# Kernel tuning notes

Hardware: AMD Instinct MI355X
Metric: run time of the kernel (lower is better)

The kernel has to match this reference:

```python
import jax, jax.numpy as jnp
import numpy as np

B, C, H, W = 64, 128, 32, 32
GROUPS = 32
EPS = 1e-6
SCALE = 0.044194173824159216  # 1/sqrt(512), as hardcoded in the torch module


def setup_inputs() -> dict:
    key = jax.random.key(0)
    ks = jax.random.split(key, 12)
    s = 1.0 / np.sqrt(C)
    return {
        "x": jax.random.normal(ks[0], (B, C, H, W), dtype=jnp.float32),
        "gn_w": jax.random.normal(ks[1], (C,), dtype=jnp.float32) * 0.02 + 1.0,
        "gn_b": jax.random.normal(ks[2], (C,), dtype=jnp.float32) * 0.02,
        "wq": jax.random.uniform(ks[3], (C, C), jnp.float32, -s, s),
        "bq": jax.random.uniform(ks[4], (C,), jnp.float32, -s, s),
        "wk": jax.random.uniform(ks[5], (C, C), jnp.float32, -s, s),
        "bk": jax.random.uniform(ks[6], (C,), jnp.float32, -s, s),
        "wv": jax.random.uniform(ks[7], (C, C), jnp.float32, -s, s),
        "bv": jax.random.uniform(ks[8], (C,), jnp.float32, -s, s),
        "wo": jax.random.uniform(ks[9], (C, C), jnp.float32, -s, s),
        "bo": jax.random.uniform(ks[10], (C,), jnp.float32, -s, s),
    }


def reference(x, gn_w, gn_b, wq, bq, wk, bk, wv, bv, wo, bo):
    b = x.shape[0]
    res = x
    # GroupNorm(32 groups, 128 channels): normalize over (channels_per_group, H, W)
    xg = x.reshape(b, GROUPS, C // GROUPS, H * W)
    mean = xg.mean(axis=(2, 3), keepdims=True)
    var = xg.var(axis=(2, 3), keepdims=True)
    xn = (xg - mean) * jax.lax.rsqrt(var + EPS)
    xn = xn.reshape(b, C, H, W) * gn_w[:, None, None] + gn_b[:, None, None]
    # flatten spatial -> sequence: [b, S=1024, C=128]
    t = xn.reshape(b, C, H * W).transpose(0, 2, 1)
    q = t @ wq.T + bq
    k = t @ wk.T + bk
    v = t @ wv.T + bv
    att = jnp.einsum('bsc,btc->bst', q, k) * SCALE  # [b, S, S]
    att = jax.nn.softmax(att, axis=-1)
    o = jnp.einsum('bst,btc->bsc', att, v)
    o = o @ wo.T + bo
    out = o.transpose(0, 2, 1).reshape(b, C, H, W) + res
    return out
```

## Files before the change

kernel.cpp:

```cpp
#include <hip/hip_runtime.h>
#include <hip/hip_bf16.h>

#define BATCH 64
#define CCH 128
#define SEQ 1024
#define NG 32
#define EPSV 1e-6f
#define SCALEV 0.044194173824159216f

typedef short v8s __attribute__((ext_vector_type(8)));
typedef short v4s __attribute__((ext_vector_type(4)));
typedef float v4f __attribute__((ext_vector_type(4)));
typedef int   v4i __attribute__((ext_vector_type(4)));
typedef unsigned short us;

__device__ __forceinline__ us f2bf(float f) {
    __hip_bfloat16 h = __float2bfloat16(f);
    return *reinterpret_cast<us*>(&h);
}

#define MFMA16(a, b, c) __builtin_amdgcn_mfma_f32_16x16x32_bf16(a, b, c, 0, 0, 0)

__device__ __forceinline__ void gld_lds16(const us* g, us* l) {
    __builtin_amdgcn_global_load_lds(
        (const __attribute__((address_space(1))) void*)g,
        (__attribute__((address_space(3))) void*)l, 16, 0, 0);
}

__global__ void prep_gn(const float* __restrict__ wq, const float* __restrict__ wk,
                        const float* __restrict__ wv, const float* __restrict__ wo,
                        us* wbf, const float* __restrict__ x,
                        float* meanr, float* rstdr) {
    int tid = threadIdx.x;
    if (blockIdx.x < 256) {
        int i = blockIdx.x * 256 + tid;
        const float* srcs[4] = {wq, wk, wv, wo};
        wbf[i] = f2bf(srcs[i >> 14][i & 16383]);
        return;
    }
    int bg = blockIdx.x - 256;
    const float4* p = (const float4*)(x + (size_t)bg * (4 * SEQ));
    float s1 = 0.f, s2 = 0.f;
    #pragma unroll
    for (int i = 0; i < 4; i++) {
        float4 v = p[i * 256 + tid];
        s1 += v.x + v.y + v.z + v.w;
        s2 += v.x * v.x + v.y * v.y + v.z * v.z + v.w * v.w;
    }
    #pragma unroll
    for (int off = 32; off; off >>= 1) {
        s1 += __shfl_down(s1, off);
        s2 += __shfl_down(s2, off);
    }
    __shared__ float a1[4], a2[4];
    int w = tid >> 6, l = tid & 63;
    if (l == 0) { a1[w] = s1; a2[w] = s2; }
    __syncthreads();
    if (tid == 0) {
        float t1 = a1[0] + a1[1] + a1[2] + a1[3];
        float t2 = a2[0] + a2[1] + a2[2] + a2[3];
        float mean = t1 * (1.0f / (4 * SEQ));
        float var  = t2 * (1.0f / (4 * SEQ)) - mean * mean;
        meanr[bg] = mean;
        rstdr[bg] = rsqrtf(var + EPSV);
    }
}

__global__ __launch_bounds__(256, 2) void qkv_kernel(
    const float* __restrict__ x, const float* __restrict__ gn_w,
    const float* __restrict__ gn_b, const float* __restrict__ meanr,
    const float* __restrict__ rstdr, const us* __restrict__ wbf,
    const float* __restrict__ bq, const float* __restrict__ bk,
    const float* __restrict__ bv,
    us* Q, us* K, us* Vt)
{
    __shared__ us tls[64 * 136];
    __shared__ float sa[CCH], sb[CCH];
    int b  = blockIdx.x >> 4;
    int s0 = (blockIdx.x & 15) * 64;
    int tid = threadIdx.x;
    const float* xb = x + (size_t)b * CCH * SEQ;

    if (tid < CCH) {
        int g = tid >> 2;
        float rs = rstdr[b * NG + g];
        float mu = meanr[b * NG + g];
        float a_ = rs * gn_w[tid];
        sa[tid] = a_;
        sb[tid] = gn_b[tid] - mu * a_;
    }
    __syncthreads();

    #pragma unroll
    for (int rep = 0; rep < 8; rep++) {
        int idx = rep * 256 + tid;
        int c = idx >> 4, s4 = idx & 15;
        float4 v = *(const float4*)&xb[c * SEQ + s0 + s4 * 4];
        float a_ = sa[c], b_ = sb[c];
        int sbase = s4 * 4;
        tls[(sbase + 0) * 136 + c] = f2bf(v.x * a_ + b_);
        tls[(sbase + 1) * 136 + c] = f2bf(v.y * a_ + b_);
        tls[(sbase + 2) * 136 + c] = f2bf(v.z * a_ + b_);
        tls[(sbase + 3) * 136 + c] = f2bf(v.w * a_ + b_);
    }
    __syncthreads();

    int w = tid >> 6, lane = tid & 63;
    int m = lane & 15, quad = lane >> 4;

    v8s bfr[6][4];
    float bias[6];
    #pragma unroll
    for (int t = 0; t < 6; t++) {
        int T = w * 6 + t;
        int o = T >> 3, ct = T & 7;
        const us* wmat = wbf + o * 16384;
        #pragma unroll
        for (int ch = 0; ch < 4; ch++)
            bfr[t][ch] = *(const v8s*)&wmat[(ct * 16 + m) * 128 + ch * 32 + quad * 8];
        const float* bb = (o == 0) ? bq : (o == 1) ? bk : bv;
        bias[t] = bb[ct * 16 + m];
    }

    us* Qb = Q + (size_t)b * SEQ * CCH;
    us* Kb = K + (size_t)b * SEQ * CCH;
    us* Vb = Vt + (size_t)b * CCH * SEQ;

    #pragma unroll
    for (int st = 0; st < 4; st++) {
        v8s a[4];
        #pragma unroll
        for (int ch = 0; ch < 4; ch++)
            a[ch] = *(const v8s*)&tls[(st * 16 + m) * 136 + ch * 32 + quad * 8];
        int srow = s0 + st * 16 + quad * 4;
        #pragma unroll
        for (int t = 0; t < 6; t++) {
            int T = w * 6 + t;
            int o = T >> 3, ct = T & 7;
            v4f acc = {0,0,0,0};
            #pragma unroll
            for (int ch = 0; ch < 4; ch++)
                acc = MFMA16(a[ch], bfr[t][ch], acc);
            int col = ct * 16 + m;
            if (o < 2) {
                us* dst = (o == 0) ? Qb : Kb;
                #pragma unroll
                for (int r = 0; r < 4; r++)
                    dst[(size_t)(srow + r) * 128 + col] = f2bf(acc[r] + bias[t]);
            } else {
                v4s pk;
                #pragma unroll
                for (int r = 0; r < 4; r++) pk[r] = (short)f2bf(acc[r] + bias[t]);
                *(v4s*)&Vb[(size_t)col * SEQ + srow] = pk;
            }
        }
    }
}

__global__ __launch_bounds__(256, 2) void attn_kernel(
    const us* __restrict__ Q, const us* __restrict__ K,
    const us* __restrict__ Vt, const us* __restrict__ wbo,
    const float* __restrict__ bo, const float* __restrict__ x,
    float* __restrict__ out)
{
    __shared__ char smem_raw[65536];

    int i = blockIdx.x;
    int b  = (i & 7) * 8 + ((i >> 3) & 7);
    int qt = i >> 6;
    int tid = threadIdx.x;
    int w = tid >> 6, lane = tid & 63;
    int m = lane & 15, quad = lane >> 4;
    int qrow0 = qt * 64 + w * 16;
    const us* Qb = Q + (size_t)b * SEQ * CCH;
    const us* Kb = K + (size_t)b * SEQ * CCH;
    const us* Vb = Vt + (size_t)b * CCH * SEQ;

    v8s aq[4];
    #pragma unroll
    for (int ch = 0; ch < 4; ch++)
        aq[ch] = *(const v8s*)&Qb[(size_t)(qrow0 + m) * 128 + ch * 32 + quad * 8];

    v4f oacc[8];
    #pragma unroll
    for (int ct = 0; ct < 8; ct++) oacc[ct] = (v4f){0, 0, 0, 0};
    float lrun = 0.f;

    const us* kg[4]; const us* vg[4];
    int jb = w * 4;
    #pragma unroll
    for (int j4 = 0; j4 < 4; j4++) {
        int j = jb + j4;
        int kr = 4 * j + (lane >> 4);
        kg[j4] = Kb + (size_t)kr * 128 + ((lane & 15) ^ (kr & 15)) * 8;
        int vc = 8 * j + (lane >> 3);
        vg[j4] = Vb + (size_t)vc * SEQ + ((lane & 7) ^ (vc & 7)) * 8;
    }
    int idx0 = 2 * (quad & 1) * 16 + m;
    int idx1 = idx0 + 16;

    #pragma unroll
    for (int j4 = 0; j4 < 4; j4++) {
        gld_lds16(kg[j4], (us*)smem_raw + (jb + j4) * 512);
        gld_lds16(vg[j4], (us*)(smem_raw + 16384) + (jb + j4) * 512);
    }

    for (int kt = 0; kt < 16; kt++) {
        int boff  = (kt & 1) ? 32768 : 0;
        int boffn = boff ^ 32768;
        __builtin_amdgcn_s_barrier();
        if (kt < 15) {
            #pragma unroll
            for (int j4 = 0; j4 < 4; j4++) {
                gld_lds16(kg[j4] + (size_t)(kt + 1) * 8192,
                          (us*)(smem_raw + boffn) + (jb + j4) * 512);
                gld_lds16(vg[j4] + (size_t)(kt + 1) * 64,
                          (us*)(smem_raw + boffn + 16384) + (jb + j4) * 512);
            }
            asm volatile("s_waitcnt vmcnt(8)" ::: "memory");
        } else {
            asm volatile("s_waitcnt vmcnt(0)" ::: "memory");
        }
        __builtin_amdgcn_s_barrier();

        const us* kl = (const us*)(smem_raw + boff);
        const us* vl = (const us*)(smem_raw + boff + 16384);

        v4f acc[4];
        __builtin_amdgcn_s_setprio(1);
        #pragma unroll
        for (int c2 = 0; c2 < 4; c2++) {
            int krow = c2 * 16 + m;
            acc[c2] = (v4f){0, 0, 0, 0};
            #pragma unroll
            for (int ch = 0; ch < 4; ch++) {
                int chunk = (ch * 4 + quad) ^ (krow & 15);
                v8s kb = *(const v8s*)&kl[krow * 128 + chunk * 8];
                acc[c2] = MFMA16(kb, aq[ch], acc[c2]);
            }
        }
        __builtin_amdgcn_s_setprio(0);

        int e[4][2];
        #pragma unroll
        for (int c2 = 0; c2 < 4; c2++) {
            float p[4];
            #pragma unroll
            for (int r = 0; r < 4; r++) {
                p[r] = __expf(acc[c2][r] * SCALEV);
                lrun += p[r];
            }
            e[c2][0] = (int)f2bf(p[0]) | ((int)f2bf(p[1]) << 16);
            e[c2][1] = (int)f2bf(p[2]) | ((int)f2bf(p[3]) << 16);
        }
        v8s pa[2];
        #pragma unroll
        for (int kc2 = 0; kc2 < 2; kc2++) {
            int c0 = (quad < 2) ? e[2 * kc2][0] : e[2 * kc2 + 1][0];
            int c1 = (quad < 2) ? e[2 * kc2][1] : e[2 * kc2 + 1][1];
            v4i t;
            t[0] = __shfl(c0, idx0);
            t[1] = __shfl(c1, idx0);
            t[2] = __shfl(c0, idx1);
            t[3] = __shfl(c1, idx1);
            pa[kc2] = __builtin_bit_cast(v8s, t);
        }
        __builtin_amdgcn_s_setprio(1);
        #pragma unroll
        for (int ct = 0; ct < 8; ct++) {
            int vrow = ct * 16 + m;
            #pragma unroll
            for (int kc2 = 0; kc2 < 2; kc2++) {
                int chunk = (kc2 * 4 + quad) ^ (vrow & 7);
                v8s vb = *(const v8s*)&vl[vrow * 64 + chunk * 8];
                oacc[ct] = MFMA16(pa[kc2], vb, oacc[ct]);
            }
        }
        __builtin_amdgcn_s_setprio(0);
    }

    float inv[4];
    {
        float rs = lrun;
        rs += __shfl_xor(rs, 16);
        rs += __shfl_xor(rs, 32);
        #pragma unroll
        for (int r = 0; r < 4; r++)
            inv[r] = 1.0f / __shfl(rs, quad * 4 + r);
    }
    __syncthreads();
    us* olds = (us*)smem_raw;
    #pragma unroll
    for (int ct = 0; ct < 8; ct++)
        #pragma unroll
        for (int r = 0; r < 4; r++)
            olds[(w * 16 + quad * 4 + r) * 136 + ct * 16 + m] =
                f2bf(oacc[ct][r] * inv[r]);
    __syncthreads();

    const float* xb = x + (size_t)b * CCH * SEQ;
    float* ob = out + (size_t)b * CCH * SEQ;
    int sbase = qt * 64 + w * 16;
    v8s obf[4];
    #pragma unroll
    for (int ch = 0; ch < 4; ch++)
        obf[ch] = *(const v8s*)&olds[(w * 16 + m) * 136 + ch * 32 + quad * 8];
    #pragma unroll
    for (int mt = 0; mt < 8; mt++) {
        v8s af[4];
        #pragma unroll
        for (int ch = 0; ch < 4; ch++)
            af[ch] = *(const v8s*)&wbo[(mt * 16 + m) * 128 + ch * 32 + quad * 8];
        v4f acc = {0,0,0,0};
        #pragma unroll
        for (int ch = 0; ch < 4; ch++)
            acc = MFMA16(af[ch], obf[ch], acc);
        #pragma unroll
        for (int r = 0; r < 4; r++) {
            int c = mt * 16 + quad * 4 + r;
            int idx = c * SEQ + sbase + m;
            ob[idx] = acc[r] + bo[c] + xb[idx];
        }
    }
}

extern "C" void kernel_launch(void* const* d_in, const int* in_sizes, int n_in,
                              void* d_out, int out_size, void* d_ws, size_t ws_size,
                              hipStream_t stream) {
    const float* x    = (const float*)d_in[0];
    const float* gn_w = (const float*)d_in[1];
    const float* gn_b = (const float*)d_in[2];
    const float* wq   = (const float*)d_in[3];
    const float* bq   = (const float*)d_in[4];
    const float* wk   = (const float*)d_in[5];
    const float* bk   = (const float*)d_in[6];
    const float* wv   = (const float*)d_in[7];
    const float* bv   = (const float*)d_in[8];
    const float* wo   = (const float*)d_in[9];
    const float* bo   = (const float*)d_in[10];
    float* out = (float*)d_out;

    char* ws = (char*)d_ws;
    us* wbf      = (us*)ws;
    float* meanr = (float*)(ws + 131072);
    float* rstdr = (float*)(ws + 139264);
    us* Qbuf     = (us*)(ws + 147456);
    us* Kbuf     = (us*)(ws + 147456 + 16777216ull);
    us* Vtbuf    = (us*)(ws + 147456 + 2ull * 16777216ull);

    prep_gn<<<256 + BATCH * NG, 256, 0, stream>>>(wq, wk, wv, wo, wbf, x, meanr, rstdr);
    qkv_kernel<<<1024, 256, 0, stream>>>(x, gn_w, gn_b, meanr, rstdr, wbf,
                                         bq, bk, bv, Qbuf, Kbuf, Vtbuf);
    attn_kernel<<<1024, 256, 0, stream>>>(Qbuf, Kbuf, Vtbuf, wbf + 3 * 16384,
                                          bo, x, out);
}
```

Baseline: 187.6 us.

## Process two 16-row query tiles per wave to reuse K/V LDS tiles

Each wave now handles 32 query rows (two 16-row subtiles) instead of 16, so each block covers 128 queries and the grid is halved. Every K and V fragment read from LDS feeds two MFMAs, which halves LDS reads and global K/V traffic per query. The output-projection epilogue reuses each loaded Wo fragment for both subtiles. In exchange, accumulator and Q register use doubles, and fewer blocks run, which may hurt occupancy and latency hiding.

```diff
diff --git a/kernel.cpp b/kernel.cpp
--- a/kernel.cpp
+++ b/kernel.cpp
@@ -171,20 +171,24 @@
     int tid = threadIdx.x;
     int w = tid >> 6, lane = tid & 63;
     int m = lane & 15, quad = lane >> 4;
-    int qrow0 = qt * 64 + w * 16;
+    int qrow0 = qt * 128 + w * 32;
     const us* Qb = Q + (size_t)b * SEQ * CCH;
     const us* Kb = K + (size_t)b * SEQ * CCH;
     const us* Vb = Vt + (size_t)b * CCH * SEQ;
 
-    v8s aq[4];
-    #pragma unroll
-    for (int ch = 0; ch < 4; ch++)
-        aq[ch] = *(const v8s*)&Qb[(size_t)(qrow0 + m) * 128 + ch * 32 + quad * 8];
-
-    v4f oacc[8];
-    #pragma unroll
-    for (int ct = 0; ct < 8; ct++) oacc[ct] = (v4f){0, 0, 0, 0};
-    float lrun = 0.f;
+    v8s aq[2][4];
+    #pragma unroll
+    for (int st = 0; st < 2; st++)
+        #pragma unroll
+        for (int ch = 0; ch < 4; ch++)
+            aq[st][ch] = *(const v8s*)&Qb[(size_t)(qrow0 + st * 16 + m) * 128 + ch * 32 + quad * 8];
+
+    v4f oacc[2][8];
+    #pragma unroll
+    for (int st = 0; st < 2; st++)
+        #pragma unroll
+        for (int ct = 0; ct < 8; ct++) oacc[st][ct] = (v4f){0, 0, 0, 0};
+    float lrun[2] = {0.f, 0.f};
 
     const us* kg[4]; const us* vg[4];
     int jb = w * 4;
@@ -226,45 +230,53 @@
         const us* kl = (const us*)(smem_raw + boff);
         const us* vl = (const us*)(smem_raw + boff + 16384);
 
-        v4f acc[4];
+        v4f acc0[4], acc1[4];
         __builtin_amdgcn_s_setprio(1);
         #pragma unroll
         for (int c2 = 0; c2 < 4; c2++) {
             int krow = c2 * 16 + m;
-            acc[c2] = (v4f){0, 0, 0, 0};
+            acc0[c2] = (v4f){0, 0, 0, 0};
+            acc1[c2] = (v4f){0, 0, 0, 0};
             #pragma unroll
             for (int ch = 0; ch < 4; ch++) {
                 int chunk = (ch * 4 + quad) ^ (krow & 15);
                 v8s kb = *(const v8s*)&kl[krow * 128 + chunk * 8];
-                acc[c2] = MFMA16(kb, aq[ch], acc[c2]);
+                acc0[c2] = MFMA16(kb, aq[0][ch], acc0[c2]);
+                acc1[c2] = MFMA16(kb, aq[1][ch], acc1[c2]);
             }
         }
         __builtin_amdgcn_s_setprio(0);
 
-        int e[4][2];
+        int e[2][4][2];
         #pragma unroll
         for (int c2 = 0; c2 < 4; c2++) {
-            float p[4];
+            float p0[4], p1[4];
             #pragma unroll
             for (int r = 0; r < 4; r++) {
-                p[r] = __expf(acc[c2][r] * SCALEV);
-                lrun += p[r];
-            }
-            e[c2][0] = (int)f2bf(p[0]) | ((int)f2bf(p[1]) << 16);
-            e[c2][1] = (int)f2bf(p[2]) | ((int)f2bf(p[3]) << 16);
-        }
-        v8s pa[2];
-        #pragma unroll
-        for (int kc2 = 0; kc2 < 2; kc2++) {
-            int c0 = (quad < 2) ? e[2 * kc2][0] : e[2 * kc2 + 1][0];
-            int c1 = (quad < 2) ? e[2 * kc2][1] : e[2 * kc2 + 1][1];
-            v4i t;
-            t[0] = __shfl(c0, idx0);
-            t[1] = __shfl(c1, idx0);
-            t[2] = __shfl(c0, idx1);
-            t[3] = __shfl(c1, idx1);
-            pa[kc2] = __builtin_bit_cast(v8s, t);
-        }
+                p0[r] = __expf(acc0[c2][r] * SCALEV);
+                p1[r] = __expf(acc1[c2][r] * SCALEV);
+                lrun[0] += p0[r];
+                lrun[1] += p1[r];
+            }
+            e[0][c2][0] = (int)f2bf(p0[0]) | ((int)f2bf(p0[1]) << 16);
+            e[0][c2][1] = (int)f2bf(p0[2]) | ((int)f2bf(p0[3]) << 16);
+            e[1][c2][0] = (int)f2bf(p1[0]) | ((int)f2bf(p1[1]) << 16);
+            e[1][c2][1] = (int)f2bf(p1[2]) | ((int)f2bf(p1[3]) << 16);
+        }
+        v8s pa[2][2];
+        #pragma unroll
+        for (int st = 0; st < 2; st++)
+            #pragma unroll
+            for (int kc2 = 0; kc2 < 2; kc2++) {
+                int c0 = (quad < 2) ? e[st][2 * kc2][0] : e[st][2 * kc2 + 1][0];
+                int c1 = (quad < 2) ? e[st][2 * kc2][1] : e[st][2 * kc2 + 1][1];
+                v4i t;
+                t[0] = __shfl(c0, idx0);
+                t[1] = __shfl(c1, idx0);
+                t[2] = __shfl(c0, idx1);
+                t[3] = __shfl(c1, idx1);
+                pa[st][kc2] = __builtin_bit_cast(v8s, t);
+            }
         __builtin_amdgcn_s_setprio(1);
         #pragma unroll
         for (int ct = 0; ct < 8; ct++) {
@@ -273,53 +285,62 @@
             for (int kc2 = 0; kc2 < 2; kc2++) {
                 int chunk = (kc2 * 4 + quad) ^ (vrow & 7);
                 v8s vb = *(const v8s*)&vl[vrow * 64 + chunk * 8];
-                oacc[ct] = MFMA16(pa[kc2], vb, oacc[ct]);
+                oacc[0][ct] = MFMA16(pa[0][kc2], vb, oacc[0][ct]);
+                oacc[1][ct] = MFMA16(pa[1][kc2], vb, oacc[1][ct]);
             }
         }
         __builtin_amdgcn_s_setprio(0);
     }
 
-    float inv[4];
-    {
-        float rs = lrun;
+    float inv[2][4];
+    #pragma unroll
+    for (int st = 0; st < 2; st++) {
+        float rs = lrun[st];
         rs += __shfl_xor(rs, 16);
         rs += __shfl_xor(rs, 32);
         #pragma unroll
         for (int r = 0; r < 4; r++)
-            inv[r] = 1.0f / __shfl(rs, quad * 4 + r);
+            inv[st][r] = 1.0f / __shfl(rs, quad * 4 + r);
     }
     __syncthreads();
     us* olds = (us*)smem_raw;
     #pragma unroll
-    for (int ct = 0; ct < 8; ct++)
-        #pragma unroll
-        for (int r = 0; r < 4; r++)
-            olds[(w * 16 + quad * 4 + r) * 136 + ct * 16 + m] =
-                f2bf(oacc[ct][r] * inv[r]);
+    for (int st = 0; st < 2; st++)
+        #pragma unroll
+        for (int ct = 0; ct < 8; ct++)
+            #pragma unroll
+            for (int r = 0; r < 4; r++)
+                olds[(w * 32 + st * 16 + quad * 4 + r) * 136 + ct * 16 + m] =
+                    f2bf(oacc[st][ct][r] * inv[st][r]);
     __syncthreads();
 
     const float* xb = x + (size_t)b * CCH * SEQ;
     float* ob = out + (size_t)b * CCH * SEQ;
-    int sbase = qt * 64 + w * 16;
-    v8s obf[4];
-    #pragma unroll
-    for (int ch = 0; ch < 4; ch++)
-        obf[ch] = *(const v8s*)&olds[(w * 16 + m) * 136 + ch * 32 + quad * 8];
+    int sbase = qt * 128 + w * 32;
+    v8s obf[2][4];
+    #pragma unroll
+    for (int st = 0; st < 2; st++)
+        #pragma unroll
+        for (int ch = 0; ch < 4; ch++)
+            obf[st][ch] = *(const v8s*)&olds[(w * 32 + st * 16 + m) * 136 + ch * 32 + quad * 8];
     #pragma unroll
     for (int mt = 0; mt < 8; mt++) {
         v8s af[4];
         #pragma unroll
         for (int ch = 0; ch < 4; ch++)
             af[ch] = *(const v8s*)&wbo[(mt * 16 + m) * 128 + ch * 32 + quad * 8];
-        v4f acc = {0,0,0,0};
-        #pragma unroll
-        for (int ch = 0; ch < 4; ch++)
-            acc = MFMA16(af[ch], obf[ch], acc);
-        #pragma unroll
-        for (int r = 0; r < 4; r++) {
-            int c = mt * 16 + quad * 4 + r;
-            int idx = c * SEQ + sbase + m;
-            ob[idx] = acc[r] + bo[c] + xb[idx];
+        #pragma unroll
+        for (int st = 0; st < 2; st++) {
+            v4f acc = {0,0,0,0};
+            #pragma unroll
+            for (int ch = 0; ch < 4; ch++)
+                acc = MFMA16(af[ch], obf[st][ch], acc);
+            #pragma unroll
+            for (int r = 0; r < 4; r++) {
+                int c = mt * 16 + quad * 4 + r;
+                int idx = c * SEQ + sbase + st * 16 + m;
+                ob[idx] = acc[r] + bo[c] + xb[idx];
+            }
         }
     }
 }
@@ -351,6 +372,6 @@
     prep_gn<<<256 + BATCH * NG, 256, 0, stream>>>(wq, wk, wv, wo, wbf, x, meanr, rstdr);
     qkv_kernel<<<1024, 256, 0, stream>>>(x, gn_w, gn_b, meanr, rstdr, wbf,
                                          bq, bk, bv, Qbuf, Kbuf, Vtbuf);
-    attn_kernel<<<1024, 256, 0, stream>>>(Qbuf, Kbuf, Vtbuf, wbf + 3 * 16384,
-                                          bo, x, out);
-}
+    attn_kernel<<<512, 256, 0, stream>>>(Qbuf, Kbuf, Vtbuf, wbf + 3 * 16384,
+                                         bo, x, out);
+}
```

New measurement: 177.5 us. 1.06x faster.
